# Kernel tuning notes

Measured on AMD Instinct MI355X. Metric: run time of the kernel, lower is better.

The kernel has to match this reference:

```python
import jax, jax.numpy as jnp
import numpy as np

BN_EPS = 1e-3
NUM_HEADS = 4
HEAD_CH = 16  # embed_channels // num_heads = 64 // 4


def _conv_bn(x, w, g, b, rm, rv, pad):
    # Conv2d (no bias) followed by eval-mode BatchNorm2d, activation=Identity.
    y = jax.lax.conv_general_dilated(
        x, w, window_strides=(1, 1), padding=[(pad, pad), (pad, pad)],
        dimension_numbers=("NCHW", "OIHW", "NCHW"))
    s = g * jax.lax.rsqrt(rv + BN_EPS)
    return y * s[None, :, None, None] + (b - rm * s)[None, :, None, None]


def setup_inputs() -> dict:
    key = jax.random.key(0)
    ks = jax.random.split(key, 16)
    B, Cin, H, W = 8, 128, 160, 160
    N, Cg, Ce, Co = 80, 512, 64, 128
    x = jax.random.normal(ks[0], (B, Cin, H, W), jnp.float32)
    guide = jax.random.normal(ks[1], (B, N, Cg), jnp.float32)
    # embed_conv (1x1) + BN params
    w_embed = jax.random.normal(ks[2], (Ce, Cin, 1, 1), jnp.float32) * 0.05
    g1 = jnp.ones((Ce,), jnp.float32)
    b1 = jnp.zeros((Ce,), jnp.float32)
    rm1 = jax.random.normal(ks[3], (Ce,), jnp.float32) * 0.1
    rv1 = jax.random.uniform(ks[4], (Ce,), jnp.float32) + 0.5
    # guide_fc
    Wg = jax.random.normal(ks[5], (Ce, Cg), jnp.float32) * 0.02
    bg = jnp.zeros((Ce,), jnp.float32)
    # per-head bias
    attn_bias = jnp.zeros((NUM_HEADS,), jnp.float32)
    # project_conv (3x3) + BN params
    w_proj = jax.random.normal(ks[6], (Co, Cin, 3, 3), jnp.float32) * 0.02
    g2 = jnp.ones((Co,), jnp.float32)
    b2 = jnp.zeros((Co,), jnp.float32)
    rm2 = jax.random.normal(ks[7], (Co,), jnp.float32) * 0.1
    rv2 = jax.random.uniform(ks[8], (Co,), jnp.float32) + 0.5
    return {"x": x, "guide": guide, "w_embed": w_embed, "g1": g1, "b1": b1,
            "rm1": rm1, "rv1": rv1, "Wg": Wg, "bg": bg, "attn_bias": attn_bias,
            "w_proj": w_proj, "g2": g2, "b2": b2, "rm2": rm2, "rv2": rv2}


def reference(x, guide, w_embed, g1, b1, rm1, rv1, Wg, bg, attn_bias,
              w_proj, g2, b2, rm2, rv2):
    B, _, H, W = x.shape
    nh, hc = NUM_HEADS, HEAD_CH
    # guide_fc -> [B, N, nh, hc]
    g = (jnp.einsum("bnc,ec->bne", guide, Wg) + bg).reshape(B, -1, nh, hc)
    # embed_conv (1x1, BN, no act) -> [B, nh, hc, H, W]
    e = _conv_bn(x, w_embed, g1, b1, rm1, rv1, 0).reshape(B, nh, hc, H, W)
    # attn: dot over head channels, max over N guides, scale, bias, sigmoid
    aw = jnp.einsum("bmchw,bnmc->bmhwn", e, g)  # [B, nh, H, W, N]
    aw = jnp.max(aw, axis=-1) * (1.0 / np.sqrt(hc)) + attn_bias[None, :, None, None]
    aw = jax.nn.sigmoid(aw)  # scale == 1.0 (with_scale=False)
    # project_conv (3x3, BN, no act), gate per-head, merge heads
    xp = _conv_bn(x, w_proj, g2, b2, rm2, rv2, 1).reshape(B, nh, -1, H, W)
    return (xp * aw[:, :, None]).reshape(B, -1, H, W)
```

## Files before the change

### kernel.cpp

```cpp
#include <hip/hip_runtime.h>
#include <hip/hip_bf16.h>
#include <stdint.h>


typedef __attribute__((ext_vector_type(8))) short short8;
typedef __attribute__((ext_vector_type(4))) float f32x4;

#define PCH2 ((size_t)8 * 162 * 176 * 32)

#define GLDS(gp, lp) __builtin_amdgcn_global_load_lds(                         \
    (const __attribute__((address_space(1))) void*)(gp),                       \
    (__attribute__((address_space(3))) void*)(lp), 16, 0, 0)

__device__ __forceinline__ unsigned short f2bf(float f) {
  unsigned int u = __float_as_uint(f);
  u += 0x7fff + ((u >> 16) & 1);
  return (unsigned short)(u >> 16);
}

__global__ __launch_bounds__(256) void k_prep_x(const float* __restrict__ x,
                                                unsigned short* __restrict__ P2) {
  __shared__ unsigned short T[8192];
  int b = blockIdx.x / 112, blk = blockIdx.x % 112;
  int tid = threadIdx.x;
  int px = blk * 256 + tid;
  int hp = px / 176, wp = px - hp * 176;
  bool interior = (px < 28512) && (hp >= 1) && (hp <= 160) && (wp >= 8) && (wp < 168);
  const float* xb = x + (size_t)b * 128 * 25600 + (hp - 1) * 160 + (wp - 8);
  int q = tid >> 2, os = tid & 3;

  for (int cs = 0; cs < 4; ++cs) {
    short8 v[4];
#pragma unroll
    for (int s = 0; s < 4; ++s) {
#pragma unroll
      for (int j = 0; j < 8; ++j) {
        float f = interior ? xb[(size_t)(cs * 32 + s * 8 + j) * 25600] : 0.f;
        v[s][j] = (short)f2bf(f);
      }
    }
    if (cs) __syncthreads();
#pragma unroll
    for (int s = 0; s < 4; ++s)
      *(short8*)(&T[(tid * 4 + (s ^ (tid & 3))) * 8]) = v[s];
    __syncthreads();
#pragma unroll
    for (int ph = 0; ph < 4; ++ph) {
      int lpx = ph * 64 + q;
      int opx = blk * 256 + lpx;
      if (opx < 28512) {
        int ohp = opx / 176, owp = opx - ohp * 176;
        size_t obase = (((size_t)b * 162 + ohp) * 176 + owp) * 32 + os * 8;
        short8 w = *(const short8*)(&T[(lpx * 4 + (os ^ (lpx & 3))) * 8]);
        *(short8*)(&P2[(size_t)cs * PCH2 + obase]) = w;
      }
    }
  }
}

__global__ __launch_bounds__(256) void k_prep_misc(
    const float* __restrict__ w_embed, const float* __restrict__ w_proj,
    const float* __restrict__ g2, const float* __restrict__ b2,
    const float* __restrict__ rm2, const float* __restrict__ rv2,
    unsigned short* __restrict__ W1t, unsigned short* __restrict__ Wpt,
    float* __restrict__ s2, float* __restrict__ t2) {
  int idx = blockIdx.x * 256 + threadIdx.x;
  if (idx < 8192) { W1t[idx] = f2bf(w_embed[idx]); return; }
  idx -= 8192;
  if (idx < 147456) {
    int cs = idx / 36864, r = idx - cs * 36864;
    int tap = r >> 12, r2 = r & 4095;
    int co = r2 >> 5, ci5 = r2 & 31;
    int ci = cs * 32 + ci5;
    Wpt[idx] = f2bf(w_proj[(co * 128 + ci) * 9 + tap]);
    return;
  }
  idx -= 147456;
  if (idx < 128) {
    float s = g2[idx] * rsqrtf(rv2[idx] + 1e-3f);
    s2[idx] = s;
    t2[idx] = b2[idx] - rm2[idx] * s;
  }
}

__global__ __launch_bounds__(64) void k_guide(
    const float* __restrict__ guide, const float* __restrict__ Wg,
    const float* __restrict__ bg, const float* __restrict__ g1,
    const float* __restrict__ b1, const float* __restrict__ rm1,
    const float* __restrict__ rv1, unsigned short* __restrict__ Gpad,
    float* __restrict__ Cst) {
  int b = blockIdx.x / 80, n = blockIdx.x % 80;
  __shared__ float gs[512];
  const float* gr = guide + ((size_t)b * 80 + n) * 512;
  for (int i = threadIdx.x; i < 512; i += 64) gs[i] = gr[i];
  __syncthreads();
  int ce = threadIdx.x;
  const float* wr = Wg + (size_t)ce * 512;
  float acc = 0.f;
  for (int k = 0; k < 512; k += 4)
    acc += gs[k] * wr[k] + gs[k + 1] * wr[k + 1] + gs[k + 2] * wr[k + 2] +
           gs[k + 3] * wr[k + 3];
  float raw = acc + bg[ce];
  float s1 = g1[ce] * rsqrtf(rv1[ce] + 1e-3f);
  float t1 = b1[ce] - rm1[ce] * s1;
  int head = ce >> 4, c = ce & 15;
  size_t gp = (((size_t)b * 4 + head) * 80 + n) * 32;
  Gpad[gp + c] = f2bf(raw * s1);
  Gpad[gp + 16 + c] = 0;
  float cp = raw * t1;
  cp += __shfl_xor(cp, 1);
  cp += __shfl_xor(cp, 2);
  cp += __shfl_xor(cp, 4);
  cp += __shfl_xor(cp, 8);
  if (c == 0) Cst[((size_t)b * 4 + head) * 80 + n] = cp;
}

__global__ __launch_bounds__(256, 4) void k_mega(
    const unsigned short* __restrict__ P2, const unsigned short* __restrict__ W1t,
    const unsigned short* __restrict__ Wpt, const unsigned short* __restrict__ Gpad,
    const float* __restrict__ Cst, const float* __restrict__ attn_bias,
    const float* __restrict__ s2, const float* __restrict__ t2,
    float* __restrict__ out) {
  __shared__ unsigned short XA[2][7680];
  __shared__ float AWL[4][64];
  int b = blockIdx.x & 7;
  int r = blockIdx.x >> 3;
  int blkN = r & 1;
  int tile = r >> 1;
  int ht = tile / 5, wt = tile - ht * 5;
  int h0 = ht * 4, w0 = wt * 32;
  int tid = threadIdx.x, lane = tid & 63, wv = tid >> 6;
  int l15 = lane & 15, l4 = lane >> 4;
  int mh = wv >> 1, nh = wv & 1;

  {
    int a2off[2];
#pragma unroll
    for (int k = 0; k < 2; ++k) {
      int c = (wv * 2 + k) * 64 + lane;
      int rr2 = c >> 7, rem = c & 127;
      int p = rem >> 2, sp = rem & 3;
      int s = sp ^ ((p >> 1) & 3);
      a2off[k] = (int)(((b * 162 + h0 + 1 + rr2) * 176 + (w0 + 8 + p)) * 32 + s * 8);
    }
    int a2base[4];
#pragma unroll
    for (int j = 0; j < 4; ++j) {
      int rr2 = mh * 2 + (j >> 1);
      int p = (j & 1) * 16 + l15;
      a2base[j] = rr2 * 128 + p * 4 + (l4 ^ ((p >> 1) & 3));
    }

    f32x4 accE[4];
#pragma unroll
    for (int j = 0; j < 4; ++j) accE[j] = (f32x4){0.f, 0.f, 0.f, 0.f};

#pragma unroll
    for (int k = 0; k < 2; ++k)
      GLDS(P2 + a2off[k], &XA[0][(wv * 2 + k) * 512]);
    __syncthreads();

#pragma unroll
    for (int cs = 0; cs < 4; ++cs) {
      if (cs < 3) {
#pragma unroll
        for (int k = 0; k < 2; ++k)
          GLDS(P2 + (size_t)(cs + 1) * PCH2 + a2off[k],
               &XA[(cs + 1) & 1][(wv * 2 + k) * 512]);
      }
      short8 BE = *(const short8*)(W1t + (blkN * 32 + nh * 16 + l15) * 128 +
                                   cs * 32 + l4 * 8);
      short8 A2[4];
#pragma unroll
      for (int j = 0; j < 4; ++j)
        A2[j] = *(const short8*)(&XA[cs & 1][a2base[j] * 8]);
#pragma unroll
      for (int j = 0; j < 4; ++j)
        accE[j] = __builtin_amdgcn_mfma_f32_16x16x32_bf16(A2[j], BE, accE[j], 0, 0, 0);
      __syncthreads();
    }

    unsigned short* Eb = &XA[0][0];
#pragma unroll
    for (int j = 0; j < 4; ++j)
#pragma unroll
      for (int rr = 0; rr < 4; ++rr) {
        int pxl = (j >> 1) * 32 + (j & 1) * 16 + l4 * 4 + rr;
        int chunk = (l15 >> 3) ^ (pxl & 1);
        Eb[wv * 1024 + pxl * 16 + chunk * 8 + (l15 & 7)] = f2bf(accE[j][rr]);
      }

    const f32x4 zf = (f32x4){0.f, 0.f, 0.f, 0.f};
    int head = blkN * 2 + nh;
    short8 Ga[5];
    f32x4 cst[5];
#pragma unroll
    for (int m5 = 0; m5 < 5; ++m5) {
      Ga[m5] = *(const short8*)(Gpad + (((size_t)b * 4 + head) * 80 + m5 * 16 + l15) * 32 + l4 * 8);
      cst[m5] = *(const f32x4*)(Cst + ((size_t)b * 4 + head) * 80 + m5 * 16 + l4 * 4);
    }
    float bias = attn_bias[head];
#pragma unroll
    for (int nt = 0; nt < 4; ++nt) {
      int pxl = nt * 16 + l15;
      int chr = (l4 & 1) ^ (pxl & 1);
      short8 Bf = *(const short8*)(&Eb[wv * 1024 + pxl * 16 + chr * 8]);
      float mx = -3.0e38f;
#pragma unroll
      for (int m5 = 0; m5 < 5; ++m5) {
        f32x4 sc = __builtin_amdgcn_mfma_f32_16x16x32_bf16(Ga[m5], Bf, zf, 0, 0, 0);
#pragma unroll
        for (int rr = 0; rr < 4; ++rr) mx = fmaxf(mx, sc[rr] + cst[m5][rr]);
      }
      mx = fmaxf(mx, __shfl_xor(mx, 16));
      mx = fmaxf(mx, __shfl_xor(mx, 32));
      if (lane < 16) AWL[wv][nt * 16 + lane] = 1.f / (1.f + __expf(-(mx * 0.25f + bias)));
    }
  }
  __syncthreads();

  size_t aoff[4];
#pragma unroll
  for (int k = 0; k < 4; ++k) {
    int i = wv * 4 + k;
    int c = i * 64 + lane;
    int cc = (c < 960) ? c : 0;
    int row = cc / 160, rem = cc - row * 160;
    int px = rem >> 2, sp = rem & 3;
    int s = sp ^ ((px >> 1) & 3);
    aoff[k] = (((size_t)b * 162 + h0 + row) * 176 + (w0 + 7 + px)) * 32 + s * 8;
  }
  int abase[2][3];
#pragma unroll
  for (int wh = 0; wh < 2; ++wh)
#pragma unroll
    for (int kx = 0; kx < 3; ++kx) {
      int px = wh * 16 + l15 + kx;
      abase[wh][kx] = px * 4 + (l4 ^ ((px >> 1) & 3));
    }
  int boff2[2];
#pragma unroll
  for (int nt = 0; nt < 2; ++nt)
    boff2[nt] = (blkN * 64 + nh * 32 + nt * 16 + l15) * 32 + l4 * 8;

  f32x4 acc[4][2];
#pragma unroll
  for (int j = 0; j < 4; ++j) {
    acc[j][0] = (f32x4){0.f, 0.f, 0.f, 0.f};
    acc[j][1] = (f32x4){0.f, 0.f, 0.f, 0.f};
  }

#pragma unroll
  for (int k = 0; k < 4; ++k) {
    int i = wv * 4 + k;
    if (i < 15) GLDS(P2 + aoff[k], &XA[0][i * 512]);
  }
  short8 Bb[3][2];
#pragma unroll
  for (int nt = 0; nt < 2; ++nt) {
    Bb[0][nt] = *(const short8*)(Wpt + boff2[nt]);
    Bb[1][nt] = *(const short8*)(Wpt + 4096 + boff2[nt]);
  }
  __syncthreads();

#pragma unroll
  for (int cs = 0; cs < 4; ++cs) {
    if (cs < 3) {
#pragma unroll
      for (int k = 0; k < 4; ++k) {
        int i = wv * 4 + k;
        if (i < 15)
          GLDS(P2 + (size_t)(cs + 1) * PCH2 + aoff[k], &XA[(cs + 1) & 1][i * 512]);
      }
    }
#pragma unroll
    for (int tap = 0; tap < 9; ++tap) {
      const int t = cs * 9 + tap;
      if (t + 2 < 36) {
#pragma unroll
        for (int nt = 0; nt < 2; ++nt)
          Bb[(t + 2) % 3][nt] =
              *(const short8*)(Wpt + (size_t)(t + 2) * 4096 + boff2[nt]);
      }
      int ky = tap / 3, kx = tap - ky * 3;
      short8 A[4];
#pragma unroll
      for (int j = 0; j < 4; ++j) {
        int rr = mh * 2 + (j >> 1) + ky;
        A[j] = *(const short8*)(&XA[cs & 1][(rr * 160 + abase[j & 1][kx]) * 8]);
      }
#pragma unroll
      for (int j = 0; j < 4; ++j)
#pragma unroll
        for (int nt = 0; nt < 2; ++nt)
          acc[j][nt] = __builtin_amdgcn_mfma_f32_16x16x32_bf16(
              A[j], Bb[t % 3][nt], acc[j][nt], 0, 0, 0);
    }
    if (cs < 3) __syncthreads();
  }

  float s2v[2], t2v[2];
#pragma unroll
  for (int nt = 0; nt < 2; ++nt) {
    int co = blkN * 64 + nh * 32 + nt * 16 + l15;
    s2v[nt] = s2[co];
    t2v[nt] = t2[co];
  }
#pragma unroll
  for (int j = 0; j < 4; ++j) {
    int h = h0 + mh * 2 + (j >> 1);
    int wbase = w0 + (j & 1) * 16 + l4 * 4;
    int pb = (j >> 1) * 32 + (j & 1) * 16 + l4 * 4;
    f32x4 a0 = *(const f32x4*)(&AWL[wv][pb]);
#pragma unroll
    for (int nt = 0; nt < 2; ++nt) {
      int co = blkN * 64 + nh * 32 + nt * 16 + l15;
      f32x4 o;
#pragma unroll
      for (int rr = 0; rr < 4; ++rr) o[rr] = (acc[j][nt][rr] * s2v[nt] + t2v[nt]) * a0[rr];
      *(f32x4*)(out + (size_t)(b * 128 + co) * 25600 + h * 160 + wbase) = o;
    }
  }
}

extern "C" void kernel_launch(void* const* d_in, const int* in_sizes, int n_in,
                              void* d_out, int out_size, void* d_ws, size_t ws_size,
                              hipStream_t stream) {
  (void)in_sizes; (void)n_in; (void)out_size; (void)ws_size;
  const float* x         = (const float*)d_in[0];
  const float* guide     = (const float*)d_in[1];
  const float* w_embed   = (const float*)d_in[2];
  const float* g1        = (const float*)d_in[3];
  const float* b1        = (const float*)d_in[4];
  const float* rm1       = (const float*)d_in[5];
  const float* rv1       = (const float*)d_in[6];
  const float* Wg        = (const float*)d_in[7];
  const float* bg        = (const float*)d_in[8];
  const float* attn_bias = (const float*)d_in[9];
  const float* w_proj    = (const float*)d_in[10];
  const float* g2        = (const float*)d_in[11];
  const float* b2        = (const float*)d_in[12];
  const float* rm2       = (const float*)d_in[13];
  const float* rv2       = (const float*)d_in[14];
  float* out = (float*)d_out;

  char* ws = (char*)d_ws;
  unsigned short* P2   = (unsigned short*)(ws);
  unsigned short* W1t  = (unsigned short*)(ws + 58392576);
  unsigned short* Wpt  = (unsigned short*)(ws + 58408960);
  unsigned short* Gpad = (unsigned short*)(ws + 58703872);
  float* Cst           = (float*)(ws + 58867712);
  float* s2            = (float*)(ws + 58877952);
  float* t2            = (float*)(ws + 58878464);

  k_prep_x<<<8 * 112, 256, 0, stream>>>(x, P2);
  k_prep_misc<<<609, 256, 0, stream>>>(w_embed, w_proj, g2, b2, rm2, rv2, W1t, Wpt, s2, t2);
  k_guide<<<640, 64, 0, stream>>>(guide, Wg, bg, g1, b1, rm1, rv1, Gpad, Cst);
  k_mega<<<3200, 256, 0, stream>>>(P2, W1t, Wpt, Gpad, Cst, attn_bias, s2, t2, out);
}
```

Measured before the change: 142.9 us.

## Remap conv MFMA warp tiling to one row per wave with all 64 channels

```diff
diff --git a/kernel.cpp b/kernel.cpp
--- a/kernel.cpp
+++ b/kernel.cpp
@@ -115,7 +115,7 @@
   if (c == 0) Cst[((size_t)b * 4 + head) * 80 + n] = cp;
 }
 
-__global__ __launch_bounds__(256, 4) void k_mega(
+__global__ __launch_bounds__(256, 3) void k_mega(
     const unsigned short* __restrict__ P2, const unsigned short* __restrict__ W1t,
     const unsigned short* __restrict__ Wpt, const unsigned short* __restrict__ Gpad,
     const float* __restrict__ Cst, const float* __restrict__ attn_bias,
@@ -238,29 +238,26 @@
       int px = wh * 16 + l15 + kx;
       abase[wh][kx] = px * 4 + (l4 ^ ((px >> 1) & 3));
     }
-  int boff2[2];
-#pragma unroll
-  for (int nt = 0; nt < 2; ++nt)
-    boff2[nt] = (blkN * 64 + nh * 32 + nt * 16 + l15) * 32 + l4 * 8;
-
-  f32x4 acc[4][2];
-#pragma unroll
-  for (int j = 0; j < 4; ++j) {
-    acc[j][0] = (f32x4){0.f, 0.f, 0.f, 0.f};
-    acc[j][1] = (f32x4){0.f, 0.f, 0.f, 0.f};
-  }
+  int boff[4];
+#pragma unroll
+  for (int nt = 0; nt < 4; ++nt)
+    boff[nt] = (blkN * 64 + nt * 16 + l15) * 32 + l4 * 8;
+
+  f32x4 acc[2][4];
+#pragma unroll
+  for (int wh = 0; wh < 2; ++wh)
+#pragma unroll
+    for (int nt = 0; nt < 4; ++nt) acc[wh][nt] = (f32x4){0.f, 0.f, 0.f, 0.f};
 
 #pragma unroll
   for (int k = 0; k < 4; ++k) {
     int i = wv * 4 + k;
     if (i < 15) GLDS(P2 + aoff[k], &XA[0][i * 512]);
   }
-  short8 Bb[3][2];
-#pragma unroll
-  for (int nt = 0; nt < 2; ++nt) {
-    Bb[0][nt] = *(const short8*)(Wpt + boff2[nt]);
-    Bb[1][nt] = *(const short8*)(Wpt + 4096 + boff2[nt]);
-  }
+  short8 Bb[2][4];
+#pragma unroll
+  for (int nt = 0; nt < 4; ++nt)
+    Bb[0][nt] = *(const short8*)(Wpt + boff[nt]);
   __syncthreads();
 
 #pragma unroll
@@ -276,48 +273,49 @@
 #pragma unroll
     for (int tap = 0; tap < 9; ++tap) {
       const int t = cs * 9 + tap;
-      if (t + 2 < 36) {
-#pragma unroll
-        for (int nt = 0; nt < 2; ++nt)
-          Bb[(t + 2) % 3][nt] =
-              *(const short8*)(Wpt + (size_t)(t + 2) * 4096 + boff2[nt]);
+      if (t + 1 < 36) {
+#pragma unroll
+        for (int nt = 0; nt < 4; ++nt)
+          Bb[(t + 1) & 1][nt] =
+              *(const short8*)(Wpt + (size_t)(t + 1) * 4096 + boff[nt]);
       }
       int ky = tap / 3, kx = tap - ky * 3;
-      short8 A[4];
-#pragma unroll
-      for (int j = 0; j < 4; ++j) {
-        int rr = mh * 2 + (j >> 1) + ky;
-        A[j] = *(const short8*)(&XA[cs & 1][(rr * 160 + abase[j & 1][kx]) * 8]);
-      }
-#pragma unroll
-      for (int j = 0; j < 4; ++j)
-#pragma unroll
-        for (int nt = 0; nt < 2; ++nt)
-          acc[j][nt] = __builtin_amdgcn_mfma_f32_16x16x32_bf16(
-              A[j], Bb[t % 3][nt], acc[j][nt], 0, 0, 0);
+      int rr = wv + ky;
+      short8 A[2];
+#pragma unroll
+      for (int wh = 0; wh < 2; ++wh)
+        A[wh] = *(const short8*)(&XA[cs & 1][(rr * 160 + abase[wh][kx]) * 8]);
+#pragma unroll
+      for (int wh = 0; wh < 2; ++wh)
+#pragma unroll
+        for (int nt = 0; nt < 4; ++nt)
+          acc[wh][nt] = __builtin_amdgcn_mfma_f32_16x16x32_bf16(
+              A[wh], Bb[t & 1][nt], acc[wh][nt], 0, 0, 0);
     }
     if (cs < 3) __syncthreads();
   }
 
-  float s2v[2], t2v[2];
-#pragma unroll
-  for (int nt = 0; nt < 2; ++nt) {
-    int co = blkN * 64 + nh * 32 + nt * 16 + l15;
+  float s2v[4], t2v[4];
+#pragma unroll
+  for (int nt = 0; nt < 4; ++nt) {
+    int co = blkN * 64 + nt * 16 + l15;
     s2v[nt] = s2[co];
     t2v[nt] = t2[co];
   }
-#pragma unroll
-  for (int j = 0; j < 4; ++j) {
-    int h = h0 + mh * 2 + (j >> 1);
-    int wbase = w0 + (j & 1) * 16 + l4 * 4;
-    int pb = (j >> 1) * 32 + (j & 1) * 16 + l4 * 4;
-    f32x4 a0 = *(const f32x4*)(&AWL[wv][pb]);
-#pragma unroll
-    for (int nt = 0; nt < 2; ++nt) {
-      int co = blkN * 64 + nh * 32 + nt * 16 + l15;
+  int h = h0 + wv;
+#pragma unroll
+  for (int wh = 0; wh < 2; ++wh) {
+    int wbase = w0 + wh * 16 + l4 * 4;
+    int pb = (wv & 1) * 32 + wh * 16 + l4 * 4;
+    f32x4 a0 = *(const f32x4*)(&AWL[(wv >> 1) * 2 + 0][pb]);
+    f32x4 a1 = *(const f32x4*)(&AWL[(wv >> 1) * 2 + 1][pb]);
+#pragma unroll
+    for (int nt = 0; nt < 4; ++nt) {
+      int co = blkN * 64 + nt * 16 + l15;
+      f32x4 g = (nt >> 1) ? a1 : a0;
       f32x4 o;
 #pragma unroll
-      for (int rr = 0; rr < 4; ++rr) o[rr] = (acc[j][nt][rr] * s2v[nt] + t2v[nt]) * a0[rr];
+      for (int rr = 0; rr < 4; ++rr) o[rr] = (acc[wh][nt][rr] * s2v[nt] + t2v[nt]) * g[rr];
       *(f32x4*)(out + (size_t)(b * 128 + co) * 25600 + h * 160 + wbase) = o;
     }
   }
```

New measurement: 189.4 us. +32.5%, slower.
